# Performance work log

Hardware: AMD Instinct MI355X
Metric: run time of the kernel (lower is better)

Reference implementation:

```python
import jax, jax.numpy as jnp
import numpy as np

V, E, H, C, T = 100000, 300, 512, 40, 4096  # vocab, embed, hidden, num_classes, seq_len


def setup_inputs() -> dict:
    key = jax.random.key(0)
    ks = jax.random.split(key, 19)
    s = lambda k, shape: jax.random.normal(k, shape, jnp.float32) * 0.05
    inp = {"x": jax.random.randint(ks[0], (T,), 0, V, dtype=jnp.int32)}
    inp["emb"] = s(ks[1], (V, E))  # frozen embedding table
    # PyTorch LSTM params, gate order (i, f, g, o); layer0 in=E, layer1 in=2H
    inp["Wih0f"] = s(ks[2], (4 * H, E)); inp["Whh0f"] = s(ks[3], (4 * H, H)); inp["b0f"] = s(ks[4], (4 * H,))
    inp["Wih0b"] = s(ks[5], (4 * H, E)); inp["Whh0b"] = s(ks[6], (4 * H, H)); inp["b0b"] = s(ks[7], (4 * H,))
    inp["Wih1f"] = s(ks[8], (4 * H, 2 * H)); inp["Whh1f"] = s(ks[9], (4 * H, H)); inp["b1f"] = s(ks[10], (4 * H,))
    inp["Wih1b"] = s(ks[11], (4 * H, 2 * H)); inp["Whh1b"] = s(ks[12], (4 * H, H)); inp["b1b"] = s(ks[13], (4 * H,))
    inp["Wc"] = s(ks[14], (C, 2 * H)); inp["bc"] = s(ks[15], (C,))
    inp["trans"] = s(ks[16], (C, C))  # CRF transitions prev->next
    inp["start"] = s(ks[17], (C,)); inp["end"] = s(ks[18], (C,))
    return inp


def _lstm_dir(x, Wih, Whh, b, reverse):
    # x: (T, D) unbatched; returns hidden states (T, H)
    Hd = Whh.shape[1]
    def step(carry, xt):
        h, c = carry
        g = xt @ Wih.T + h @ Whh.T + b  # (4H,)
        i, f, gg, o = jnp.split(g, 4)
        i = jax.nn.sigmoid(i); f = jax.nn.sigmoid(f)
        gg = jnp.tanh(gg); o = jax.nn.sigmoid(o)
        c = f * c + i * gg
        h = o * jnp.tanh(c)
        return (h, c), h
    xs = x[::-1] if reverse else x
    init = (jnp.zeros((Hd,), x.dtype), jnp.zeros((Hd,), x.dtype))
    _, hs = jax.lax.scan(step, init, xs)
    return hs[::-1] if reverse else hs


def _viterbi(emissions, trans, start, end):
    # emissions: (T, C); returns best path (T,) int32
    def fwd(score, em):
        m = score[:, None] + trans  # (C_prev, C_next)
        bp = jnp.argmax(m, axis=0).astype(jnp.int32)
        return jnp.max(m, axis=0) + em, bp
    score0 = start + emissions[0]
    final, bps = jax.lax.scan(fwd, score0, emissions[1:])  # bps: (T-1, C)
    last = jnp.argmax(final + end).astype(jnp.int32)
    def back(tag, bp):
        prev = bp[tag]
        return prev, prev
    _, path = jax.lax.scan(back, last, bps, reverse=True)  # tags 0..T-2 in order
    return jnp.concatenate([path, last[None]])


def reference(x, emb, Wih0f, Whh0f, b0f, Wih0b, Whh0b, b0b, Wih1f, Whh1f, b1f, Wih1b, Whh1b, b1b, Wc, bc, trans, start, end):
    e = emb[x]  # (T, E); dropout is identity at eval
    h0 = jnp.concatenate([_lstm_dir(e, Wih0f, Whh0f, b0f, False),
                          _lstm_dir(e, Wih0b, Whh0b, b0b, True)], axis=-1)  # (T, 2H)
    h1 = jnp.concatenate([_lstm_dir(h0, Wih1f, Whh1f, b1f, False),
                          _lstm_dir(h0, Wih1b, Whh1b, b1b, True)], axis=-1)  # (T, 2H)
    o = h1 @ Wc.T + bc  # (T, C)
    tag_scores = jax.nn.log_softmax(o, axis=1)
    tags = _viterbi(tag_scores, trans, start, end)
    return tag_scores, tags
```

## Files before the change

### kernel.cpp

```cpp
#include <hip/hip_runtime.h>


typedef unsigned int u32;
typedef unsigned long long u64;
typedef u32 u32x4 __attribute__((ext_vector_type(4)));
typedef __attribute__((ext_vector_type(8))) short s16x8;
typedef __attribute__((ext_vector_type(4))) float f32x4;

#define TT 4096
#define HH 512
#define CC 40
#define NG 2048

__device__ __forceinline__ float sigm(float x) { return 1.0f / (1.0f + __expf(-x)); }
__device__ __forceinline__ float tanh_(float x) { return 1.0f - 2.0f / (__expf(2.0f * x) + 1.0f); }

__device__ __forceinline__ void st_sys_u32(u32* p, u32 v) {
    asm volatile("global_store_dword %0, %1, off sc0 sc1"
                 :
                 : "v"(p), "v"(v)
                 : "memory");
}

__device__ __forceinline__ void ld_mall_b256(const float* p, u32x4& r0, u32x4& r1) {
    asm volatile(
        "global_load_dwordx4 %0, %2, off sc0 sc1\n\t"
        "global_load_dwordx4 %1, %2, off offset:16 sc0 sc1\n\t"
        "s_waitcnt vmcnt(0)"
        : "=&v"(r0), "=&v"(r1)
        : "v"(p)
        : "memory");
}

__device__ __forceinline__ void split_pack8(const float* f, s16x8& hi, s16x8& lo) {
#pragma unroll
    for (int j = 0; j < 8; j++) {
        float x = f[j];
        u32 h = __float_as_uint(x) & 0xFFFF0000u;
        float hf = __uint_as_float(h);
        hi[j] = (short)(h >> 16);
        lo[j] = (short)(__float_as_uint(x - hf) >> 16);
    }
}

__global__ __launch_bounds__(256, 2) void gemm_bf16s_k(const float* __restrict__ A0,
                                                       const float* __restrict__ A1,
                                                       const int* __restrict__ xidx,
                                                       const float* __restrict__ W0,
                                                       const float* __restrict__ bias0,
                                                       float* __restrict__ C0,
                                                       const float* __restrict__ W1,
                                                       const float* __restrict__ bias1,
                                                       float* __restrict__ C1,
                                                       int M, int N, int K, int Ksplit) {
    __shared__ __align__(16) short sAh[128 * 32];
    __shared__ __align__(16) short sAl[128 * 32];
    __shared__ __align__(16) short sWh[128 * 32];
    __shared__ __align__(16) short sWl[128 * 32];
    const int tid = threadIdx.x;
    const int bn = blockIdx.x, bm = blockIdx.y;
    const float* W    = blockIdx.z ? W1 : W0;
    const float* bias = blockIdx.z ? bias1 : bias0;
    float*       C    = blockIdx.z ? C1 : C0;
    const int wid = tid >> 6, lane = tid & 63;
    const int qm = (wid >> 1) * 64, qn = (wid & 1) * 64;
    const int fr = lane & 15, fq = lane >> 4;

    const int srow = tid >> 1;
    const int kh = (tid & 1) * 16;

    const int am = bm * 128 + srow;
    const float* arow = xidx ? (A0 + (size_t)xidx[am] * K) : nullptr;
    const float* a0r = xidx ? nullptr : (A0 + (size_t)am * Ksplit);
    const float* a1r = xidx ? nullptr : (A1 + (size_t)am * Ksplit);
    const float* wrow = W + (size_t)(bn * 128 + srow) * K;

    f32x4 acc[4][4] = {};

    auto LOADP = [&](int kp, float* fa, float* fw) {
        const int kb = kp * 32 + kh;
        if (kb + 16 <= K) {
#pragma unroll
            for (int j = 0; j < 16; j += 4) {
                int k = kb + j;
                const float* s = xidx ? (arow + k)
                                      : ((k < Ksplit) ? (a0r + k) : (a1r + (k - Ksplit)));
                float4 v = *(const float4*)s;
                fa[j] = v.x; fa[j + 1] = v.y; fa[j + 2] = v.z; fa[j + 3] = v.w;
                float4 wv = *(const float4*)(wrow + k);
                fw[j] = wv.x; fw[j + 1] = wv.y; fw[j + 2] = wv.z; fw[j + 3] = wv.w;
            }
        } else {
#pragma unroll
            for (int j = 0; j < 16; j++) {
                int k = kb + j;
                float av = 0.f, wv = 0.f;
                if (k < K) {
                    av = xidx ? arow[k] : ((k < Ksplit) ? a0r[k] : a1r[k - Ksplit]);
                    wv = wrow[k];
                }
                fa[j] = av; fw[j] = wv;
            }
        }
    };

    float fa[16], fw[16];
    LOADP(0, fa, fw);

    const int NP = (K + 31) >> 5;
    for (int kp = 0; kp < NP; kp++) {
        s16x8 hA[2], lA[2], hW[2], lW[2];
#pragma unroll
        for (int c = 0; c < 2; c++) {
            split_pack8(fa + c * 8, hA[c], lA[c]);
            split_pack8(fw + c * 8, hW[c], lW[c]);
        }
        __syncthreads();
#pragma unroll
        for (int c = 0; c < 2; c++) {
            int ch = (tid & 1) * 2 + c;
            int pch = ch ^ ((srow >> 1) & 3);
            int off = srow * 32 + pch * 8;
            *(s16x8*)&sAh[off] = hA[c];
            *(s16x8*)&sAl[off] = lA[c];
            *(s16x8*)&sWh[off] = hW[c];
            *(s16x8*)&sWl[off] = lW[c];
        }
        __syncthreads();

        if (kp + 1 < NP) LOADP(kp + 1, fa, fw);

        s16x8 ah[4], al[4];
#pragma unroll
        for (int m = 0; m < 4; m++) {
            int row = qm + m * 16 + fr;
            int off = row * 32 + ((fq ^ ((row >> 1) & 3)) * 8);
            ah[m] = *(const s16x8*)&sAh[off];
            al[m] = *(const s16x8*)&sAl[off];
        }
#pragma unroll
        for (int n = 0; n < 4; n++) {
            int row = qn + n * 16 + fr;
            int off = row * 32 + ((fq ^ ((row >> 1) & 3)) * 8);
            s16x8 bh = *(const s16x8*)&sWh[off];
            s16x8 bl = *(const s16x8*)&sWl[off];
#pragma unroll
            for (int m = 0; m < 4; m++) {
                acc[m][n] = __builtin_amdgcn_mfma_f32_16x16x32_bf16(ah[m], bh, acc[m][n], 0, 0, 0);
                acc[m][n] = __builtin_amdgcn_mfma_f32_16x16x32_bf16(ah[m], bl, acc[m][n], 0, 0, 0);
                acc[m][n] = __builtin_amdgcn_mfma_f32_16x16x32_bf16(al[m], bh, acc[m][n], 0, 0, 0);
            }
        }
    }

#pragma unroll
    for (int n = 0; n < 4; n++) {
        int gcol = bn * 128 + qn + n * 16 + fr;
        float b = bias[gcol];
#pragma unroll
        for (int m = 0; m < 4; m++) {
            int rbase = bm * 128 + qm + m * 16 + fq * 4;
#pragma unroll
            for (int r2 = 0; r2 < 4; r2++)
                C[(size_t)(rbase + r2) * N + gcol] = acc[m][n][r2] + b;
        }
    }
}

__global__ __attribute__((amdgpu_flat_work_group_size(512, 512), amdgpu_waves_per_eu(2, 2)))
void lstm_phase_k(const float* __restrict__ WxF,
                  const float* __restrict__ WxB,
                  const float* __restrict__ WhhF,
                  const float* __restrict__ WhhB,
                  float* __restrict__ histF,
                  float* __restrict__ histB,
                  int phase) {
    const int wg = blockIdx.x & 31;
    const int dir = blockIdx.x >> 5;
    const int tid = threadIdx.x;
    const float* Wx = dir ? WxB : WxF;
    const float* Whh = dir ? WhhB : WhhF;
    float* hist = dir ? histB : histF;
    const u32 ENC = phase ? 0x7F800000u : 0u;

    const int r = tid >> 3, seg = tid & 7;
    const int grow = (r >> 4) * 512 + wg * 16 + (r & 15);

    float w[64];
    {
        const float* wr = Whh + (size_t)grow * HH + seg * 64;
#pragma unroll
        for (int i = 0; i < 16; i++) {
            float4 v = *(const float4*)(wr + i * 4);
            w[i * 4 + 0] = v.x; w[i * 4 + 1] = v.y; w[i * 4 + 2] = v.z; w[i * 4 + 3] = v.w;
        }
    }

    const int j = (tid < 62) ? (tid + (tid >= wg * 2 ? 2 : 0)) : 0;

    __shared__ float lds_h[8 * 68];
    __shared__ float lds_g[64];
    float c_state = 0.f;
    int capped = 0;

    for (int s = 0; s < TT; ++s) {
        const int t = dir ? (TT - 1 - s) : s;
        float wxv = 0.f;
        if (seg == 0) wxv = Wx[(size_t)t * NG + grow];

        if (s > 0) {
            const int tprev = dir ? (t + 1) : (t - 1);
            if (tid < 62) {
                const float* p = hist + (size_t)tprev * HH + j * 8;
                u32x4 v0, v1;
                if (!capped) {
                    int it = 0;
                    for (;;) {
                        ld_mall_b256(p, v0, v1);
                        bool ok;
                        if (phase) {
                            ok = ((v0.x & 0x7F800000u) >= 0x40000000u) &&
                                 ((v0.y & 0x7F800000u) >= 0x40000000u) &&
                                 ((v0.z & 0x7F800000u) >= 0x40000000u) &&
                                 ((v0.w & 0x7F800000u) >= 0x40000000u) &&
                                 ((v1.x & 0x7F800000u) >= 0x40000000u) &&
                                 ((v1.y & 0x7F800000u) >= 0x40000000u) &&
                                 ((v1.z & 0x7F800000u) >= 0x40000000u) &&
                                 ((v1.w & 0x7F800000u) >= 0x40000000u);
                        } else {
                            ok = (v0.x != 0xAAAAAAAAu) && (v0.y != 0xAAAAAAAAu) &&
                                 (v0.z != 0xAAAAAAAAu) && (v0.w != 0xAAAAAAAAu) &&
                                 (v1.x != 0xAAAAAAAAu) && (v1.y != 0xAAAAAAAAu) &&
                                 (v1.z != 0xAAAAAAAAu) && (v1.w != 0xAAAAAAAAu);
                        }
                        if (ok) break;
                        if (++it > (1 << 18)) { capped = 1; break; }
                    }
                } else {
                    ld_mall_b256(p, v0, v1);
                }
                float* dst = &lds_h[(j >> 3) * 68 + ((j & 7) * 8)];
                float4 f0, f1;
                f0.x = __uint_as_float(v0.x ^ ENC); f0.y = __uint_as_float(v0.y ^ ENC);
                f0.z = __uint_as_float(v0.z ^ ENC); f0.w = __uint_as_float(v0.w ^ ENC);
                f1.x = __uint_as_float(v1.x ^ ENC); f1.y = __uint_as_float(v1.y ^ ENC);
                f1.z = __uint_as_float(v1.z ^ ENC); f1.w = __uint_as_float(v1.w ^ ENC);
                *(float4*)dst = f0;
                *(float4*)(dst + 4) = f1;
            }
            __syncthreads();
            float a0 = 0.f, a1 = 0.f, a2 = 0.f, a3 = 0.f;
            const float4* hv4 = (const float4*)&lds_h[seg * 68];
#pragma unroll
            for (int i = 0; i < 16; i++) {
                float4 hv = hv4[i];
                a0 += w[i * 4 + 0] * hv.x;
                a1 += w[i * 4 + 1] * hv.y;
                a2 += w[i * 4 + 2] * hv.z;
                a3 += w[i * 4 + 3] * hv.w;
            }
            float acc = (a0 + a1) + (a2 + a3);
            acc += __shfl_xor(acc, 1);
            acc += __shfl_xor(acc, 2);
            acc += __shfl_xor(acc, 4);
            if (seg == 0) lds_g[r] = acc + wxv;
        } else {
            if (seg == 0) lds_g[r] = wxv;
        }
        __syncthreads();

        if (tid < 16) {
            float gi = lds_g[tid], gf = lds_g[16 + tid], gg = lds_g[32 + tid], go = lds_g[48 + tid];
            float iv = sigm(gi), fv = sigm(gf), gv = tanh_(gg), ov = sigm(go);
            c_state = fv * c_state + iv * gv;
            float h = ov * tanh_(c_state);
            int hidx = wg * 16 + tid;
            lds_h[(hidx >> 6) * 68 + (hidx & 63)] = h;
            st_sys_u32((u32*)&hist[(size_t)t * HH + hidx], __float_as_uint(h) ^ ENC);
        }
    }
}

__global__ __launch_bounds__(64, 4) void classifier_k(const float* __restrict__ histF,
                                                      const float* __restrict__ histB,
                                                      const float* __restrict__ Wc,
                                                      const float* __restrict__ bc,
                                                      float* __restrict__ outsc) {
    int t = blockIdx.x, lane = threadIdx.x;
    __shared__ float hrow[1024];
    const uint4* hf4 = (const uint4*)(histF + (size_t)t * HH);
    const uint4* hb4 = (const uint4*)(histB + (size_t)t * HH);
#pragma unroll
    for (int jj = 0; jj < 4; jj++) {
        int idx4 = jj * 64 + lane;
        uint4 u = (idx4 < 128) ? hf4[idx4] : hb4[idx4 - 128];
        u.x ^= 0x7F800000u; u.y ^= 0x7F800000u; u.z ^= 0x7F800000u; u.w ^= 0x7F800000u;
        float4 v;
        v.x = __uint_as_float(u.x); v.y = __uint_as_float(u.y);
        v.z = __uint_as_float(u.z); v.w = __uint_as_float(u.w);
        *(float4*)&hrow[idx4 * 4] = v;
    }
    __syncthreads();
    float o = 0.f;
    if (lane < CC) {
        o = bc[lane];
        const float4* wr = (const float4*)(Wc + (size_t)lane * 1024);
#pragma unroll 4
        for (int kk = 0; kk < 256; ++kk) {
            float4 w4 = wr[kk];
            float4 h4 = *(const float4*)&hrow[kk * 4];
            o += w4.x * h4.x + w4.y * h4.y + w4.z * h4.z + w4.w * h4.w;
        }
    }
    float m = (lane < CC) ? o : -1e30f;
#pragma unroll
    for (int d = 1; d < 64; d <<= 1) m = fmaxf(m, __shfl_xor(m, d));
    float ex = (lane < CC) ? __expf(o - m) : 0.f;
#pragma unroll
    for (int d = 1; d < 64; d <<= 1) ex += __shfl_xor(ex, d);
    float lse = m + __logf(ex);
    if (lane < CC) outsc[(size_t)t * CC + lane] = o - lse;
}

__global__ __launch_bounds__(64) void viterbi_k(const float* __restrict__ em,
                                               const float* __restrict__ trans,
                                               const float* __restrict__ startv,
                                               const float* __restrict__ endv,
                                               unsigned char* __restrict__ bp,
                                               float* __restrict__ outtags) {
    int lane = threadIdx.x;
    float tcol[CC];
#pragma unroll
    for (int p = 0; p < CC; p++) tcol[p] = 0.f;
    if (lane < CC) {
#pragma unroll
        for (int p = 0; p < CC; p++) tcol[p] = trans[p * CC + lane];
    }
    float s = (lane < CC) ? (startv[lane] + em[lane]) : 0.f;

    for (int t = 1; t < TT; ++t) {
        float emv = (lane < CC) ? em[(size_t)t * CC + lane] : 0.f;
        float b0 = -1e30f, b1 = -1e30f;
        int i0 = 0, i1 = 20;
#pragma unroll
        for (int p = 0; p < 20; p++) {
            float c0 = __shfl(s, p) + tcol[p];
            float c1 = __shfl(s, p + 20) + tcol[p + 20];
            if (c0 > b0) { b0 = c0; i0 = p; }
            if (c1 > b1) { b1 = c1; i1 = p + 20; }
        }
        float best = b0; int bi = i0;
        if (b1 > b0) { best = b1; bi = i1; }
        s = best + emv;
        if (lane < CC) bp[(size_t)t * CC + lane] = (unsigned char)bi;
    }
    float fv = (lane < CC) ? (s + endv[lane]) : -1e30f;
    int fi = (lane < CC) ? lane : 63;
#pragma unroll
    for (int d = 1; d < 64; d <<= 1) {
        float ov = __shfl_xor(fv, d);
        int oi = __shfl_xor(fi, d);
        if (ov > fv || (ov == fv && oi < fi)) { fv = ov; fi = oi; }
    }
    __threadfence();
    if (lane == 0) {
        int cur = fi;
        outtags[TT - 1] = (float)cur;
        for (int t = TT - 2; t >= 0; --t) {
            cur = bp[(size_t)(t + 1) * CC + cur];
            outtags[t] = (float)cur;
        }
    }
}

extern "C" void kernel_launch(void* const* d_in, const int* in_sizes, int n_in,
                              void* d_out, int out_size, void* d_ws, size_t ws_size,
                              hipStream_t stream) {
    const int*   x     = (const int*)d_in[0];
    const float* emb   = (const float*)d_in[1];
    const float* Wih0f = (const float*)d_in[2];
    const float* Whh0f = (const float*)d_in[3];
    const float* b0f   = (const float*)d_in[4];
    const float* Wih0b = (const float*)d_in[5];
    const float* Whh0b = (const float*)d_in[6];
    const float* b0b   = (const float*)d_in[7];
    const float* Wih1f = (const float*)d_in[8];
    const float* Whh1f = (const float*)d_in[9];
    const float* b1f   = (const float*)d_in[10];
    const float* Wih1b = (const float*)d_in[11];
    const float* Whh1b = (const float*)d_in[12];
    const float* b1b   = (const float*)d_in[13];
    const float* Wc    = (const float*)d_in[14];
    const float* bc    = (const float*)d_in[15];
    const float* trans = (const float*)d_in[16];
    const float* startv= (const float*)d_in[17];
    const float* endv  = (const float*)d_in[18];

    char* ws = (char*)d_ws;
    unsigned char* bp = (unsigned char*)(ws + 1024);
    float* WxF  = (float*)(ws + 262144);
    float* WxB  = (float*)(ws + 33816576);
    float* histF= (float*)(ws + 67371008);
    float* histB= (float*)(ws + 75759616);

    if (ws_size < (size_t)84148224) return;

    float* out_sc   = (float*)d_out;
    float* out_tags = out_sc + (size_t)TT * CC;

    gemm_bf16s_k<<<dim3(16, 32, 2), 256, 0, stream>>>(emb, nullptr, x,
                                                      Wih0f, b0f, WxF, Wih0b, b0b, WxB,
                                                      TT, NG, 300, 300);
    lstm_phase_k<<<64, 512, 0, stream>>>(WxF, WxB, Whh0f, Whh0b, histF, histB, 0);
    gemm_bf16s_k<<<dim3(16, 32, 2), 256, 0, stream>>>(histF, histB, nullptr,
                                                      Wih1f, b1f, WxF, Wih1b, b1b, WxB,
                                                      TT, NG, 1024, 512);
    lstm_phase_k<<<64, 512, 0, stream>>>(WxF, WxB, Whh1f, Whh1b, histF, histB, 1);
    classifier_k<<<TT, 64, 0, stream>>>(histF, histB, Wc, bc, out_sc);
    viterbi_k<<<1, 64, 0, stream>>>(out_sc, trans, startv, endv, bp, out_tags);
}
```

Before: 17.25 ms.

## Split Viterbi into max-only forward, parallel chunked backpointers, and chunk walk

Measured after the change: 16.42 ms. 4.8% less time.

```diff
diff --git a/kernel.cpp b/kernel.cpp
--- a/kernel.cpp
+++ b/kernel.cpp
@@ -322,37 +322,42 @@
     if (lane < CC) outsc[(size_t)t * CC + lane] = o - lse;
 }
 
-__global__ __launch_bounds__(64) void viterbi_k(const float* __restrict__ em,
-                                               const float* __restrict__ trans,
-                                               const float* __restrict__ startv,
-                                               const float* __restrict__ endv,
-                                               unsigned char* __restrict__ bp,
-                                               float* __restrict__ outtags) {
-    int lane = threadIdx.x;
+__global__ __launch_bounds__(64) void vit_fwd_k(const float* __restrict__ em,
+                                                const float* __restrict__ trans,
+                                                const float* __restrict__ startv,
+                                                const float* __restrict__ endv,
+                                                float* __restrict__ s_all,
+                                                u32* __restrict__ fi_out) {
+    const int lane = threadIdx.x;
     float tcol[CC];
 #pragma unroll
-    for (int p = 0; p < CC; p++) tcol[p] = 0.f;
-    if (lane < CC) {
-#pragma unroll
-        for (int p = 0; p < CC; p++) tcol[p] = trans[p * CC + lane];
-    }
-    float s = (lane < CC) ? (startv[lane] + em[lane]) : 0.f;
-
-    for (int t = 1; t < TT; ++t) {
-        float emv = (lane < CC) ? em[(size_t)t * CC + lane] : 0.f;
-        float b0 = -1e30f, b1 = -1e30f;
-        int i0 = 0, i1 = 20;
-#pragma unroll
-        for (int p = 0; p < 20; p++) {
-            float c0 = __shfl(s, p) + tcol[p];
-            float c1 = __shfl(s, p + 20) + tcol[p + 20];
-            if (c0 > b0) { b0 = c0; i0 = p; }
-            if (c1 > b1) { b1 = c1; i1 = p + 20; }
-        }
-        float best = b0; int bi = i0;
-        if (b1 > b0) { best = b1; bi = i1; }
-        s = best + emv;
-        if (lane < CC) bp[(size_t)t * CC + lane] = (unsigned char)bi;
+    for (int p = 0; p < CC; p++) tcol[p] = (lane < CC) ? trans[p * CC + lane] : -1e30f;
+    __shared__ __align__(16) float srow[CC];
+    float s = (lane < CC) ? (startv[lane] + em[lane]) : -1e30f;
+    if (lane < CC) { s_all[lane] = s; srow[lane] = s; }
+    float emv = (lane < CC) ? em[(size_t)1 * CC + lane] : 0.f;
+    for (int t = 1; t < TT; t++) {
+        float c[CC];
+        const float4* sr4 = (const float4*)srow;
+#pragma unroll
+        for (int q = 0; q < 10; q++) {
+            float4 sv = sr4[q];
+            c[q * 4 + 0] = sv.x + tcol[q * 4 + 0];
+            c[q * 4 + 1] = sv.y + tcol[q * 4 + 1];
+            c[q * 4 + 2] = sv.z + tcol[q * 4 + 2];
+            c[q * 4 + 3] = sv.w + tcol[q * 4 + 3];
+        }
+        float emn = (t + 1 < TT && lane < CC) ? em[(size_t)(t + 1) * CC + lane] : 0.f;
+#pragma unroll
+        for (int i = 0; i < 20; i++) c[i] = fmaxf(c[i], c[i + 20]);
+#pragma unroll
+        for (int i = 0; i < 10; i++) c[i] = fmaxf(c[i], c[i + 10]);
+#pragma unroll
+        for (int i = 0; i < 5; i++) c[i] = fmaxf(c[i], c[i + 5]);
+        float m = fmaxf(fmaxf(fmaxf(c[0], c[1]), fmaxf(c[2], c[3])), c[4]);
+        s = m + emv;
+        emv = emn;
+        if (lane < CC) { srow[lane] = s; s_all[(size_t)t * CC + lane] = s; }
     }
     float fv = (lane < CC) ? (s + endv[lane]) : -1e30f;
     int fi = (lane < CC) ? lane : 63;
@@ -362,14 +367,70 @@
         int oi = __shfl_xor(fi, d);
         if (ov > fv || (ov == fv && oi < fi)) { fv = ov; fi = oi; }
     }
-    __threadfence();
-    if (lane == 0) {
-        int cur = fi;
-        outtags[TT - 1] = (float)cur;
-        for (int t = TT - 2; t >= 0; --t) {
-            cur = bp[(size_t)(t + 1) * CC + cur];
-            outtags[t] = (float)cur;
-        }
+    if (lane == 0) fi_out[0] = (u32)fi;
+}
+
+__global__ __launch_bounds__(64) void vit_chunk_k(const float* __restrict__ s_all,
+                                                  const float* __restrict__ trans,
+                                                  u32* __restrict__ tbl) {
+    const int c = blockIdx.x, lane = threadIdx.x;
+    const int tlo = c * 16;
+    __shared__ float sld[16][CC];
+    __shared__ unsigned char bpl[16][CC];
+    for (int idx = lane; idx < 16 * CC; idx += 64) {
+        int row = idx / CC, col = idx % CC;
+        int t = tlo - 1 + row;
+        sld[row][col] = (t >= 0) ? s_all[(size_t)t * CC + col] : 0.f;
+    }
+    float tcol[CC];
+#pragma unroll
+    for (int p = 0; p < CC; p++) tcol[p] = (lane < CC) ? trans[p * CC + lane] : 0.f;
+    __syncthreads();
+    if (lane < CC) {
+        for (int i = (c == 0 ? 1 : 0); i < 16; i++) {
+            float b = -1e30f; int bi = 0;
+#pragma unroll
+            for (int p = 0; p < CC; p++) {
+                float v = sld[i][p] + tcol[p];
+                if (v > b) { b = v; bi = p; }
+            }
+            bpl[i][lane] = (unsigned char)bi;
+        }
+    }
+    __syncthreads();
+    if (lane < CC) {
+        unsigned char pth[16];
+        int cur = lane;
+        pth[15] = (unsigned char)cur;
+        for (int i = 14; i >= 0; i--) { cur = bpl[i + 1][cur]; pth[i] = (unsigned char)cur; }
+        u32 entry = (c > 0) ? (u32)bpl[0][cur] : 0u;
+        u32* row = tbl + ((size_t)c * CC + lane) * 5;
+#pragma unroll
+        for (int q = 0; q < 4; q++)
+            row[q] = (u32)pth[q * 4] | ((u32)pth[q * 4 + 1] << 8) |
+                     ((u32)pth[q * 4 + 2] << 16) | ((u32)pth[q * 4 + 3] << 24);
+        row[4] = entry;
+    }
+}
+
+__global__ __launch_bounds__(64) void vit_walk_k(const u32* __restrict__ tbl,
+                                                 const u32* __restrict__ fi_in,
+                                                 float* __restrict__ outtags) {
+    if (threadIdx.x != 0) return;
+    int cur = (int)fi_in[0];
+    for (int c = (TT / 16) - 1; c >= 0; c--) {
+        const u32* row = tbl + ((size_t)c * CC + cur) * 5;
+        u32 p0 = row[0], p1 = row[1], p2 = row[2], p3 = row[3];
+        cur = (int)row[4];
+        float* o = outtags + c * 16;
+        o[0]  = (float)(p0 & 255); o[1]  = (float)((p0 >> 8) & 255);
+        o[2]  = (float)((p0 >> 16) & 255); o[3]  = (float)(p0 >> 24);
+        o[4]  = (float)(p1 & 255); o[5]  = (float)((p1 >> 8) & 255);
+        o[6]  = (float)((p1 >> 16) & 255); o[7]  = (float)(p1 >> 24);
+        o[8]  = (float)(p2 & 255); o[9]  = (float)((p2 >> 8) & 255);
+        o[10] = (float)((p2 >> 16) & 255); o[11] = (float)(p2 >> 24);
+        o[12] = (float)(p3 & 255); o[13] = (float)((p3 >> 8) & 255);
+        o[14] = (float)((p3 >> 16) & 255); o[15] = (float)(p3 >> 24);
     }
 }
 
@@ -397,11 +458,13 @@
     const float* endv  = (const float*)d_in[18];
 
     char* ws = (char*)d_ws;
-    unsigned char* bp = (unsigned char*)(ws + 1024);
     float* WxF  = (float*)(ws + 262144);
     float* WxB  = (float*)(ws + 33816576);
     float* histF= (float*)(ws + 67371008);
     float* histB= (float*)(ws + 75759616);
+    float* s_all = (float*)(ws + 262144);
+    u32*   vtbl  = (u32*)(ws + 262144 + 655360);
+    u32*   fi_ws = (u32*)(ws + 262144 + 655360 + 204800);
 
     if (ws_size < (size_t)84148224) return;
 
@@ -417,5 +480,7 @@
                                                       TT, NG, 1024, 512);
     lstm_phase_k<<<64, 512, 0, stream>>>(WxF, WxB, Whh1f, Whh1b, histF, histB, 1);
     classifier_k<<<TT, 64, 0, stream>>>(histF, histB, Wc, bc, out_sc);
-    viterbi_k<<<1, 64, 0, stream>>>(out_sc, trans, startv, endv, bp, out_tags);
-}
+    vit_fwd_k<<<1, 64, 0, stream>>>(out_sc, trans, startv, endv, s_all, fi_ws);
+    vit_chunk_k<<<TT / 16, 64, 0, stream>>>(s_all, trans, vtbl);
+    vit_walk_k<<<1, 64, 0, stream>>>(vtbl, fi_ws, out_tags);
+}
```
